# Performance work log

Measured on AMD Instinct MI355X. Metric: run time of the kernel, lower is better.

The kernel has to match this reference:

```python
import jax, jax.numpy as jnp
import numpy as np
import math

B, T, D, N = 4, 2048, 1024, 16
HD = D // N
SCALE = math.sqrt(D)  # source scales by sqrt(d_key) = sqrt(full model dim)
BIG = 1e9

def setup_inputs() -> dict:
    key = jax.random.key(0)
    ks = jax.random.split(key, 11)
    s = 1.0 / math.sqrt(D)
    return {
        "query": jax.random.normal(ks[0], (B, T, D), jnp.float32),
        "key": jax.random.normal(ks[1], (B, T, D), jnp.float32),
        "value": jax.random.normal(ks[2], (B, T, D), jnp.float32),
        "wq_w": jax.random.normal(ks[3], (D, D), jnp.float32) * s,
        "wq_b": jnp.zeros((D,), jnp.float32),
        "wk_w": jax.random.normal(ks[4], (D, D), jnp.float32) * s,
        "wk_b": jnp.zeros((D,), jnp.float32),
        "wv_w": jax.random.normal(ks[5], (D, D), jnp.float32) * s,
        "wv_b": jnp.zeros((D,), jnp.float32),
        "wo_w": jax.random.normal(ks[6], (D, D), jnp.float32) * s,
        "wo_b": jnp.zeros((D,), jnp.float32),
    }

def reference(query, key, value, wq_w, wq_b, wk_w, wk_b, wv_w, wv_b, wo_w, wo_b):
    # projections (torch Linear equiv; weights stored as (in,out))
    q = query @ wq_w + wq_b
    k = key @ wk_w + wk_b
    v = value @ wv_w + wv_b
    # split heads: (B,T,D) -> (B,N,T,HD)
    def split(x):
        return x.reshape(B, T, N, HD).transpose(0, 2, 1, 3)
    q, k, v = split(q), split(k), split(v)
    # dot products (source does elementwise mul+sum == einsum)
    scores = jnp.einsum('bnqd,bnkd->bnqk', q, k)
    # only_attend_front: subtract 1e9 on strict upper triangle
    tri = jnp.triu(jnp.ones((T, T), scores.dtype), 1) * BIG
    scores = scores - tri
    logits = scores / SCALE
    probs = jax.nn.softmax(logits, axis=-1)
    # zero rows where every position is masked (source trick)
    alive = ((scores <= -BIG / 2).sum(-1, keepdims=True) < T).astype(probs.dtype)
    probs = probs * alive
    out = jnp.einsum('bnqk,bnkd->bnqd', probs, v)  # (B,N,T,HD)
    out = out.transpose(0, 2, 1, 3).reshape(B, T, D)
    return out @ wo_w + wo_b
```

## Files before the change

kernel.cpp:

```cpp
#include <hip/hip_runtime.h>
#include <hip/hip_bf16.h>

#define BB 4
#define TT 2048
#define DD 1024
#define NHEAD 16
#define HDIM 64

typedef __bf16 v8bf __attribute__((ext_vector_type(8)));
typedef __bf16 v4bf __attribute__((ext_vector_type(4)));
typedef float  v4f  __attribute__((ext_vector_type(4)));

#define C2SCALE 0.04508422376f

__device__ __forceinline__ void gl2lds16(const void* g, void* l) {
  __builtin_amdgcn_global_load_lds(
      (__attribute__((address_space(1))) const void*)g,
      (__attribute__((address_space(3))) void*)l, 16, 0, 0);
}

__global__ __launch_bounds__(256) void prep(
    const float* __restrict__ qsrc, const float* __restrict__ ksrc,
    const float* __restrict__ vsrc,
    const float* __restrict__ w0, const float* __restrict__ w1,
    const float* __restrict__ w2, const float* __restrict__ w3,
    __bf16* __restrict__ qdst, __bf16* __restrict__ kdst,
    __bf16* __restrict__ vdst,
    __bf16* __restrict__ t0, __bf16* __restrict__ t1,
    __bf16* __restrict__ t2, __bf16* __restrict__ t3) {
  constexpr int STR = 72;
  __shared__ __bf16 sh[64 * STR];
  int bx = blockIdx.x, tid = threadIdx.x;
  if (bx < 1536) {
    int z = bx >> 9, ib = bx & 511;
    const float* src = z == 0 ? qsrc : z == 1 ? ksrc : vsrc;
    __bf16* dst = z == 0 ? qdst : z == 1 ? kdst : vdst;
#pragma unroll
    for (int k = 0; k < 8; ++k) {
      int u = ib * 2048 + k * 256 + tid;
      const float4* s = (const float4*)src + (size_t)u * 2;
      float4 f0 = s[0], f1 = s[1];
      v8bf v;
      v[0] = (__bf16)f0.x; v[1] = (__bf16)f0.y; v[2] = (__bf16)f0.z; v[3] = (__bf16)f0.w;
      v[4] = (__bf16)f1.x; v[5] = (__bf16)f1.y; v[6] = (__bf16)f1.z; v[7] = (__bf16)f1.w;
      *(v8bf*)(dst + (size_t)u * 8) = v;
    }
  } else {
    int idx = bx - 1536;
    int z = idx >> 8;
    const float* W = z == 0 ? w0 : z == 1 ? w1 : z == 2 ? w2 : w3;
    __bf16* Wt = z == 0 ? t0 : z == 1 ? t1 : z == 2 ? t2 : t3;
    int n0 = (idx & 15) * 64, k0 = ((idx >> 4) & 15) * 64;
#pragma unroll
    for (int p = 0; p < 4; ++p) {
      int c = tid + p * 256;
      int r = c >> 4, off = (c & 15) * 4;
      float4 f = *(const float4*)(W + (size_t)(k0 + r) * DD + n0 + off);
      __bf16* d = &sh[r * STR + off];
      d[0] = (__bf16)f.x; d[1] = (__bf16)f.y; d[2] = (__bf16)f.z; d[3] = (__bf16)f.w;
    }
    __syncthreads();
#pragma unroll
    for (int p = 0; p < 2; ++p) {
      int c = tid + p * 256;
      int nr = c >> 3, koff = (c & 7) * 8;
      v8bf v;
#pragma unroll
      for (int j = 0; j < 8; ++j) v[j] = sh[(koff + j) * STR + nr];
      *(v8bf*)(Wt + (size_t)(n0 + nr) * DD + k0 + koff) = v;
    }
  }
}

__device__ __forceinline__ void gemm_core(const __bf16* __restrict__ A,
                                          const __bf16* __restrict__ Wt,
                                          int m0, int n0,
                                          __bf16* ash, __bf16* bsh,
                                          int wave, int lane, int quad, int l15,
                                          v4f acc[4][4]) {
  int wm = (wave & 1) * 64, wn = (wave >> 1) * 64;
  for (int k0 = 0; k0 < DD; k0 += 64) {
    __syncthreads();
#pragma unroll
    for (int i = 0; i < 4; ++i) {
      int c = wave * 256 + i * 64 + lane;
      int row = c >> 3, g = (c & 7) ^ (row & 7);
      gl2lds16(A + (size_t)(m0 + row) * DD + k0 + g * 8, ash + wave * 2048 + i * 512);
      gl2lds16(Wt + (size_t)(n0 + row) * DD + k0 + g * 8, bsh + wave * 2048 + i * 512);
    }
    __syncthreads();
#pragma unroll
    for (int ks = 0; ks < 2; ++ks) {
      int sw = (((ks * 4 + quad) ^ (l15 & 7))) * 8;
      v8bf a[4], b[4];
#pragma unroll
      for (int jm = 0; jm < 4; ++jm) a[jm] = *(v8bf*)&ash[(wm + jm * 16 + l15) * 64 + sw];
#pragma unroll
      for (int jn = 0; jn < 4; ++jn) b[jn] = *(v8bf*)&bsh[(wn + jn * 16 + l15) * 64 + sw];
#pragma unroll
      for (int jm = 0; jm < 4; ++jm)
#pragma unroll
        for (int jn = 0; jn < 4; ++jn)
          acc[jm][jn] = __builtin_amdgcn_mfma_f32_16x16x32_bf16(a[jm], b[jn], acc[jm][jn], 0, 0, 0);
    }
  }
}

__device__ __forceinline__ void swz_tiles(int& m0, int& n0) {
  int lin = blockIdx.x + 8 * blockIdx.y;
  int c = lin & 7, t = lin >> 3;
  n0 = (t & 7) * 128;
  m0 = (c + ((t >> 3) << 3)) * 128;
}

__global__ __launch_bounds__(256) void gemm_qkv(
    const __bf16* __restrict__ Qc, const __bf16* __restrict__ Kc,
    const __bf16* __restrict__ Vc,
    const __bf16* __restrict__ wqT, const __bf16* __restrict__ wkT,
    const __bf16* __restrict__ wvT,
    const float* __restrict__ qb, const float* __restrict__ kb,
    const float* __restrict__ vb,
    __bf16* __restrict__ Qp, __bf16* __restrict__ Kp, __bf16* __restrict__ VTb) {
  __shared__ __bf16 ash[128 * 64];
  __shared__ __bf16 bsh[128 * 64];
  int z = blockIdx.z;
  const __bf16* A  = z == 0 ? Qc : z == 1 ? Kc : Vc;
  const __bf16* Wt = z == 0 ? wqT : z == 1 ? wkT : wvT;
  const float* bias = z == 0 ? qb : z == 1 ? kb : vb;
  int tid = threadIdx.x, wave = tid >> 6, lane = tid & 63;
  int quad = lane >> 4, l15 = lane & 15;
  int m0, n0;
  swz_tiles(m0, n0);
  int wm = (wave & 1) * 64, wn = (wave >> 1) * 64;
  v4f acc[4][4];
#pragma unroll
  for (int jm = 0; jm < 4; ++jm)
#pragma unroll
    for (int jn = 0; jn < 4; ++jn) acc[jm][jn] = (v4f){0.f, 0.f, 0.f, 0.f};

  gemm_core(A, Wt, m0, n0, ash, bsh, wave, lane, quad, l15, acc);

  if (z == 2) {
    int b = m0 >> 11;
    int tbase = (m0 & 2047) + wm;
#pragma unroll
    for (int jn = 0; jn < 4; ++jn) {
      int col = n0 + wn + jn * 16 + l15;
      float bv = bias[col];
      __bf16* rowp = VTb + ((size_t)(b * 16 + (col >> 6)) * 64 + (col & 63)) * TT;
#pragma unroll
      for (int jm = 0; jm < 4; ++jm) {
        v4bf o;
#pragma unroll
        for (int r = 0; r < 4; ++r) o[r] = (__bf16)(acc[jm][jn][r] + bv);
        *(v4bf*)(rowp + tbase + jm * 16 + quad * 4) = o;
      }
    }
  } else {
    __bf16* C = z == 0 ? Qp : Kp;
    float scale = z == 0 ? C2SCALE : 1.0f;
#pragma unroll
    for (int jn = 0; jn < 4; ++jn) {
      int col = n0 + wn + jn * 16 + l15;
      float bv = bias[col];
#pragma unroll
      for (int jm = 0; jm < 4; ++jm) {
#pragma unroll
        for (int r = 0; r < 4; ++r) {
          int row = m0 + wm + jm * 16 + quad * 4 + r;
          C[(size_t)row * DD + col] = (__bf16)((acc[jm][jn][r] + bv) * scale);
        }
      }
    }
  }
}

__global__ __launch_bounds__(256) void gemm_out(const __bf16* __restrict__ A,
                                                const __bf16* __restrict__ Wt,
                                                const float* __restrict__ bias,
                                                float* __restrict__ C) {
  __shared__ __bf16 ash[128 * 64];
  __shared__ __bf16 bsh[128 * 64];
  int tid = threadIdx.x, wave = tid >> 6, lane = tid & 63;
  int quad = lane >> 4, l15 = lane & 15;
  int m0, n0;
  swz_tiles(m0, n0);
  int wm = (wave & 1) * 64, wn = (wave >> 1) * 64;
  v4f acc[4][4];
#pragma unroll
  for (int jm = 0; jm < 4; ++jm)
#pragma unroll
    for (int jn = 0; jn < 4; ++jn) acc[jm][jn] = (v4f){0.f, 0.f, 0.f, 0.f};

  gemm_core(A, Wt, m0, n0, ash, bsh, wave, lane, quad, l15, acc);

#pragma unroll
  for (int jn = 0; jn < 4; ++jn) {
    int col = n0 + wn + jn * 16 + l15;
    float bv = bias[col];
#pragma unroll
    for (int jm = 0; jm < 4; ++jm) {
#pragma unroll
      for (int r = 0; r < 4; ++r) {
        int row = m0 + wm + jm * 16 + quad * 4 + r;
        C[(size_t)row * DD + col] = acc[jm][jn][r] + bv;
      }
    }
  }
}

__global__ __launch_bounds__(256) void attn_bal(const __bf16* __restrict__ Q,
                                                const __bf16* __restrict__ K,
                                                const __bf16* __restrict__ VT,
                                                __bf16* __restrict__ O) {
  __shared__ __bf16 ksh[2][64 * 64];
  __shared__ __bf16 vsh[2][64 * 64];
  __shared__ __bf16 psh[128 * 64];
  int tid = threadIdx.x, wave = tid >> 6, lane = tid & 63;
  int quad = lane >> 4, l15 = lane & 15;
  int swz = l15 & 7;
  int c = blockIdx.x;
  int by = blockIdx.y;
  int bh = c + 8 * (by & 7);
  int qi = 15 - (by >> 3);
  int b = bh >> 4, h = bh & 15;
  const __bf16* Qb = Q + (size_t)(b * TT) * DD + h * HDIM;
  const __bf16* Kb = K + (size_t)(b * TT) * DD + h * HDIM;
  const __bf16* Vb = VT + (size_t)bh * HDIM * TT;
  __bf16* Ob = O + (size_t)(b * TT) * DD + h * HDIM;

  v8bf ones;
#pragma unroll
  for (int j = 0; j < 8; ++j) ones[j] = (__bf16)1.0f;

  int q0 = qi * 128;
  int ktiles = 2 * qi + 2;

#pragma unroll
  for (int i = 0; i < 4; ++i) {
    int cc = wave * 256 + i * 64 + lane;
    int row = cc >> 3, g = (cc & 7) ^ (row & 7);
    gl2lds16(Qb + (size_t)(q0 + row) * DD + g * 8, psh + wave * 2048 + i * 512);
  }
#pragma unroll
  for (int i = 0; i < 2; ++i) {
    int cc = wave * 128 + i * 64 + lane;
    int row = cc >> 3, g = (cc & 7) ^ (row & 7);
    gl2lds16(Kb + (size_t)row * DD + g * 8, &ksh[0][wave * 1024 + i * 512]);
    gl2lds16(Vb + (size_t)row * TT + g * 8, &vsh[0][wave * 1024 + i * 512]);
  }
  __builtin_amdgcn_s_waitcnt(0);
  __syncthreads();

  v8bf qf[2][2];
#pragma unroll
  for (int set = 0; set < 2; ++set)
#pragma unroll
    for (int ks = 0; ks < 2; ++ks)
      qf[set][ks] = *(v8bf*)&psh[(wave * 32 + set * 16 + l15) * 64 + ((ks * 4 + quad) ^ swz) * 8];

  int qg[2] = {q0 + wave * 32 + l15, q0 + wave * 32 + 16 + l15};
  v4f oacc[2][4], lracc[2];
#pragma unroll
  for (int set = 0; set < 2; ++set) {
    lracc[set] = (v4f){0.f, 0.f, 0.f, 0.f};
#pragma unroll
    for (int jm = 0; jm < 4; ++jm) oacc[set][jm] = (v4f){0.f, 0.f, 0.f, 0.f};
  }

  int pbuf = 0;
  for (int kt = 0; kt < ktiles; ++kt) {
    if (kt + 1 < ktiles) {
      int k0n = (kt + 1) * 64;
#pragma unroll
      for (int i = 0; i < 2; ++i) {
        int cc = wave * 128 + i * 64 + lane;
        int row = cc >> 3, g = (cc & 7) ^ (row & 7);
        gl2lds16(Kb + (size_t)(k0n + row) * DD + g * 8, &ksh[pbuf ^ 1][wave * 1024 + i * 512]);
        gl2lds16(Vb + (size_t)row * TT + k0n + g * 8, &vsh[pbuf ^ 1][wave * 1024 + i * 512]);
      }
    }
    int k0 = kt * 64;
    const __bf16* kshp = &ksh[pbuf][0];
    const __bf16* vshp = &vsh[pbuf][0];

    v4f s[2][4];
#pragma unroll
    for (int set = 0; set < 2; ++set)
#pragma unroll
      for (int jf = 0; jf < 4; ++jf) s[set][jf] = (v4f){0.f, 0.f, 0.f, 0.f};
    __builtin_amdgcn_s_setprio(1);
#pragma unroll
    for (int ks = 0; ks < 2; ++ks) {
      int sw = ((ks * 4 + quad) ^ swz) * 8;
#pragma unroll
      for (int jf = 0; jf < 4; ++jf) {
        v8bf kf = *(v8bf*)&kshp[(jf * 16 + l15) * 64 + sw];
        s[0][jf] = __builtin_amdgcn_mfma_f32_16x16x32_bf16(kf, qf[0][ks], s[0][jf], 0, 0, 0);
        s[1][jf] = __builtin_amdgcn_mfma_f32_16x16x32_bf16(kf, qf[1][ks], s[1][jf], 0, 0, 0);
      }
    }
    __builtin_amdgcn_s_setprio(0);

    bool diag = (kt >= 2 * qi);
#pragma unroll
    for (int set = 0; set < 2; ++set) {
      int qrow = wave * 32 + set * 16 + l15;
      __bf16* prow = &psh[qrow * 64];
#pragma unroll
      for (int jf = 0; jf < 4; ++jf) {
        v4bf pk;
#pragma unroll
        for (int r = 0; r < 4; ++r) {
          float p = __builtin_amdgcn_exp2f(s[set][jf][r]);
          if (diag) {
            int kg = k0 + jf * 16 + quad * 4 + r;
            if (kg > qg[set]) p = 0.f;
          }
          pk[r] = (__bf16)p;
        }
        int chunk = jf * 2 + (quad >> 1);
        *(v4bf*)&prow[(chunk ^ swz) * 8 + (quad & 1) * 4] = pk;
      }
    }

    __builtin_amdgcn_s_setprio(1);
#pragma unroll
    for (int ks = 0; ks < 2; ++ks) {
      int sw = ((ks * 4 + quad) ^ swz) * 8;
      v8bf pb0 = *(v8bf*)&psh[(wave * 32 + l15) * 64 + sw];
      v8bf pb1 = *(v8bf*)&psh[(wave * 32 + 16 + l15) * 64 + sw];
      lracc[0] = __builtin_amdgcn_mfma_f32_16x16x32_bf16(ones, pb0, lracc[0], 0, 0, 0);
      lracc[1] = __builtin_amdgcn_mfma_f32_16x16x32_bf16(ones, pb1, lracc[1], 0, 0, 0);
#pragma unroll
      for (int jm = 0; jm < 4; ++jm) {
        v8bf vf = *(v8bf*)&vshp[(jm * 16 + l15) * 64 + sw];
        oacc[0][jm] = __builtin_amdgcn_mfma_f32_16x16x32_bf16(vf, pb0, oacc[0][jm], 0, 0, 0);
        oacc[1][jm] = __builtin_amdgcn_mfma_f32_16x16x32_bf16(vf, pb1, oacc[1][jm], 0, 0, 0);
      }
    }
    __builtin_amdgcn_s_setprio(0);

    __builtin_amdgcn_s_waitcnt(0);
    __syncthreads();
    pbuf ^= 1;
  }

#pragma unroll
  for (int set = 0; set < 2; ++set) {
    float inv = 1.0f / lracc[set][0];
    int q = q0 + wave * 32 + set * 16 + l15;
#pragma unroll
    for (int jm = 0; jm < 4; ++jm) {
      v4bf o;
#pragma unroll
      for (int r = 0; r < 4; ++r) o[r] = (__bf16)(oacc[set][jm][r] * inv);
      *(v4bf*)(Ob + (size_t)q * DD + jm * 16 + quad * 4) = o;
    }
  }
}

extern "C" void kernel_launch(void* const* d_in, const int* in_sizes, int n_in,
                              void* d_out, int out_size, void* d_ws, size_t ws_size,
                              hipStream_t stream) {
  const float* query = (const float*)d_in[0];
  const float* key_  = (const float*)d_in[1];
  const float* value = (const float*)d_in[2];
  const float* wq_w = (const float*)d_in[3];
  const float* wq_b = (const float*)d_in[4];
  const float* wk_w = (const float*)d_in[5];
  const float* wk_b = (const float*)d_in[6];
  const float* wv_w = (const float*)d_in[7];
  const float* wv_b = (const float*)d_in[8];
  const float* wo_w = (const float*)d_in[9];
  const float* wo_b = (const float*)d_in[10];

  char* ws = (char*)d_ws;
  const size_t MB = (size_t)1 << 20;
  __bf16* wqT = (__bf16*)(ws + 0 * MB);
  __bf16* wkT = (__bf16*)(ws + 2 * MB);
  __bf16* wvT = (__bf16*)(ws + 4 * MB);
  __bf16* woT = (__bf16*)(ws + 6 * MB);
  __bf16* Qc  = (__bf16*)(ws + 8 * MB);
  __bf16* Kc  = (__bf16*)(ws + 24 * MB);
  __bf16* Vc  = (__bf16*)(ws + 40 * MB);
  __bf16* Qp  = (__bf16*)(ws + 56 * MB);
  __bf16* Kp  = (__bf16*)(ws + 72 * MB);
  __bf16* VTb = (__bf16*)(ws + 88 * MB);
  __bf16* Ab  = (__bf16*)(ws + 8 * MB);
  float* out = (float*)d_out;

  dim3 tb(256);
  prep<<<dim3(2560), tb, 0, stream>>>(query, key_, value, wq_w, wk_w, wv_w, wo_w,
                                      Qc, Kc, Vc, wqT, wkT, wvT, woT);
  gemm_qkv<<<dim3(8, 64, 3), tb, 0, stream>>>(Qc, Kc, Vc, wqT, wkT, wvT,
                                              wq_b, wk_b, wv_b, Qp, Kp, VTb);
  attn_bal<<<dim3(8, 128), tb, 0, stream>>>(Qp, Kp, VTb, Ab);
  gemm_out<<<dim3(8, 64), tb, 0, stream>>>(Ab, woT, wo_b, out);
}
```

Measured before the change: 308.2 us.

## Enlarge attention query tile to 256 rows per block with dynamic LDS

The attention kernel now processes 256 query rows per block instead of 128, so each wave handles 64 rows (four 16-row sets). Each K/V tile loaded into LDS is reused across twice as many queries. The grid is halved and the query-tile ordering changes to alternate long and short causal rows. The kernel moves to 64KB of dynamic shared memory with a launch bound of two blocks per CU. This raises register and LDS pressure and leaves fewer blocks to balance the causal work.

```diff
diff --git a/kernel.cpp b/kernel.cpp
--- a/kernel.cpp
+++ b/kernel.cpp
@@ -209,20 +209,22 @@
   }
 }
 
-__global__ __launch_bounds__(256) void attn_bal(const __bf16* __restrict__ Q,
-                                                const __bf16* __restrict__ K,
-                                                const __bf16* __restrict__ VT,
-                                                __bf16* __restrict__ O) {
-  __shared__ __bf16 ksh[2][64 * 64];
-  __shared__ __bf16 vsh[2][64 * 64];
-  __shared__ __bf16 psh[128 * 64];
+__global__ __launch_bounds__(256, 2) void attn_bal(const __bf16* __restrict__ Q,
+                                                   const __bf16* __restrict__ K,
+                                                   const __bf16* __restrict__ VT,
+                                                   __bf16* __restrict__ O) {
+  extern __shared__ __bf16 lds[];
+  __bf16* ksh = lds;
+  __bf16* vsh = lds + 8192;
+  __bf16* psh = lds + 16384;
   int tid = threadIdx.x, wave = tid >> 6, lane = tid & 63;
   int quad = lane >> 4, l15 = lane & 15;
   int swz = l15 & 7;
   int c = blockIdx.x;
-  int by = blockIdx.y;
-  int bh = c + 8 * (by & 7);
-  int qi = 15 - (by >> 3);
+  int y = blockIdx.y;
+  int bh = c + 8 * (y & 7);
+  int yy = y >> 3;
+  int qi = yy < 4 ? 7 - yy : yy - 4;
   int b = bh >> 4, h = bh & 15;
   const __bf16* Qb = Q + (size_t)(b * TT) * DD + h * HDIM;
   const __bf16* Kb = K + (size_t)(b * TT) * DD + h * HDIM;
@@ -233,36 +235,38 @@
 #pragma unroll
   for (int j = 0; j < 8; ++j) ones[j] = (__bf16)1.0f;
 
-  int q0 = qi * 128;
-  int ktiles = 2 * qi + 2;
-
-#pragma unroll
-  for (int i = 0; i < 4; ++i) {
-    int cc = wave * 256 + i * 64 + lane;
+  int q0 = qi * 256;
+  int ktiles = 4 * qi + 4;
+
+#pragma unroll
+  for (int i = 0; i < 8; ++i) {
+    int cc = wave * 512 + i * 64 + lane;
     int row = cc >> 3, g = (cc & 7) ^ (row & 7);
-    gl2lds16(Qb + (size_t)(q0 + row) * DD + g * 8, psh + wave * 2048 + i * 512);
+    gl2lds16(Qb + (size_t)(q0 + row) * DD + g * 8, psh + wave * 4096 + i * 512);
   }
 #pragma unroll
   for (int i = 0; i < 2; ++i) {
     int cc = wave * 128 + i * 64 + lane;
     int row = cc >> 3, g = (cc & 7) ^ (row & 7);
-    gl2lds16(Kb + (size_t)row * DD + g * 8, &ksh[0][wave * 1024 + i * 512]);
-    gl2lds16(Vb + (size_t)row * TT + g * 8, &vsh[0][wave * 1024 + i * 512]);
+    gl2lds16(Kb + (size_t)row * DD + g * 8, ksh + wave * 1024 + i * 512);
+    gl2lds16(Vb + (size_t)row * TT + g * 8, vsh + wave * 1024 + i * 512);
   }
   __builtin_amdgcn_s_waitcnt(0);
   __syncthreads();
 
-  v8bf qf[2][2];
-#pragma unroll
-  for (int set = 0; set < 2; ++set)
+  v8bf qf[4][2];
+#pragma unroll
+  for (int set = 0; set < 4; ++set)
 #pragma unroll
     for (int ks = 0; ks < 2; ++ks)
-      qf[set][ks] = *(v8bf*)&psh[(wave * 32 + set * 16 + l15) * 64 + ((ks * 4 + quad) ^ swz) * 8];
-
-  int qg[2] = {q0 + wave * 32 + l15, q0 + wave * 32 + 16 + l15};
-  v4f oacc[2][4], lracc[2];
-#pragma unroll
-  for (int set = 0; set < 2; ++set) {
+      qf[set][ks] = *(v8bf*)&psh[(wave * 64 + set * 16 + l15) * 64 + ((ks * 4 + quad) ^ swz) * 8];
+
+  int qg[4];
+#pragma unroll
+  for (int set = 0; set < 4; ++set) qg[set] = q0 + wave * 64 + set * 16 + l15;
+  v4f oacc[4][4], lracc[4];
+#pragma unroll
+  for (int set = 0; set < 4; ++set) {
     lracc[set] = (v4f){0.f, 0.f, 0.f, 0.f};
 #pragma unroll
     for (int jm = 0; jm < 4; ++jm) oacc[set][jm] = (v4f){0.f, 0.f, 0.f, 0.f};
@@ -276,51 +280,63 @@
       for (int i = 0; i < 2; ++i) {
         int cc = wave * 128 + i * 64 + lane;
         int row = cc >> 3, g = (cc & 7) ^ (row & 7);
-        gl2lds16(Kb + (size_t)(k0n + row) * DD + g * 8, &ksh[pbuf ^ 1][wave * 1024 + i * 512]);
-        gl2lds16(Vb + (size_t)row * TT + k0n + g * 8, &vsh[pbuf ^ 1][wave * 1024 + i * 512]);
+        gl2lds16(Kb + (size_t)(k0n + row) * DD + g * 8,
+                 ksh + (pbuf ^ 1) * 4096 + wave * 1024 + i * 512);
+        gl2lds16(Vb + (size_t)row * TT + k0n + g * 8,
+                 vsh + (pbuf ^ 1) * 4096 + wave * 1024 + i * 512);
       }
     }
     int k0 = kt * 64;
-    const __bf16* kshp = &ksh[pbuf][0];
-    const __bf16* vshp = &vsh[pbuf][0];
-
-    v4f s[2][4];
-#pragma unroll
-    for (int set = 0; set < 2; ++set)
-#pragma unroll
-      for (int jf = 0; jf < 4; ++jf) s[set][jf] = (v4f){0.f, 0.f, 0.f, 0.f};
-    __builtin_amdgcn_s_setprio(1);
+    const __bf16* kshp = ksh + pbuf * 4096;
+    const __bf16* vshp = vsh + pbuf * 4096;
+
+    v8bf kf[2][4];
 #pragma unroll
     for (int ks = 0; ks < 2; ++ks) {
       int sw = ((ks * 4 + quad) ^ swz) * 8;
 #pragma unroll
-      for (int jf = 0; jf < 4; ++jf) {
-        v8bf kf = *(v8bf*)&kshp[(jf * 16 + l15) * 64 + sw];
-        s[0][jf] = __builtin_amdgcn_mfma_f32_16x16x32_bf16(kf, qf[0][ks], s[0][jf], 0, 0, 0);
-        s[1][jf] = __builtin_amdgcn_mfma_f32_16x16x32_bf16(kf, qf[1][ks], s[1][jf], 0, 0, 0);
-      }
-    }
-    __builtin_amdgcn_s_setprio(0);
-
-    bool diag = (kt >= 2 * qi);
-#pragma unroll
-    for (int set = 0; set < 2; ++set) {
-      int qrow = wave * 32 + set * 16 + l15;
-      __bf16* prow = &psh[qrow * 64];
-#pragma unroll
-      for (int jf = 0; jf < 4; ++jf) {
-        v4bf pk;
-#pragma unroll
-        for (int r = 0; r < 4; ++r) {
-          float p = __builtin_amdgcn_exp2f(s[set][jf][r]);
-          if (diag) {
-            int kg = k0 + jf * 16 + quad * 4 + r;
-            if (kg > qg[set]) p = 0.f;
+      for (int jf = 0; jf < 4; ++jf)
+        kf[ks][jf] = *(v8bf*)&kshp[(jf * 16 + l15) * 64 + sw];
+    }
+
+    bool diag = (kt >= 4 * qi);
+#pragma unroll
+    for (int sp = 0; sp < 2; ++sp) {
+      v4f s[2][4];
+#pragma unroll
+      for (int ss = 0; ss < 2; ++ss)
+#pragma unroll
+        for (int jf = 0; jf < 4; ++jf) s[ss][jf] = (v4f){0.f, 0.f, 0.f, 0.f};
+      __builtin_amdgcn_s_setprio(1);
+#pragma unroll
+      for (int ks = 0; ks < 2; ++ks)
+#pragma unroll
+        for (int jf = 0; jf < 4; ++jf) {
+          s[0][jf] = __builtin_amdgcn_mfma_f32_16x16x32_bf16(kf[ks][jf], qf[sp * 2][ks], s[0][jf], 0, 0, 0);
+          s[1][jf] = __builtin_amdgcn_mfma_f32_16x16x32_bf16(kf[ks][jf], qf[sp * 2 + 1][ks], s[1][jf], 0, 0, 0);
+        }
+      __builtin_amdgcn_s_setprio(0);
+
+#pragma unroll
+      for (int ss = 0; ss < 2; ++ss) {
+        int set = sp * 2 + ss;
+        int qrow = wave * 64 + set * 16 + l15;
+        __bf16* prow = &psh[qrow * 64];
+#pragma unroll
+        for (int jf = 0; jf < 4; ++jf) {
+          v4bf pk;
+#pragma unroll
+          for (int r = 0; r < 4; ++r) {
+            float p = __builtin_amdgcn_exp2f(s[ss][jf][r]);
+            if (diag) {
+              int kg = k0 + jf * 16 + quad * 4 + r;
+              if (kg > qg[set]) p = 0.f;
+            }
+            pk[r] = (__bf16)p;
           }
-          pk[r] = (__bf16)p;
+          int chunk = jf * 2 + (quad >> 1);
+          *(v4bf*)&prow[(chunk ^ swz) * 8 + (quad & 1) * 4] = pk;
         }
-        int chunk = jf * 2 + (quad >> 1);
-        *(v4bf*)&prow[(chunk ^ swz) * 8 + (quad & 1) * 4] = pk;
       }
     }
 
@@ -328,15 +344,19 @@
 #pragma unroll
     for (int ks = 0; ks < 2; ++ks) {
       int sw = ((ks * 4 + quad) ^ swz) * 8;
-      v8bf pb0 = *(v8bf*)&psh[(wave * 32 + l15) * 64 + sw];
-      v8bf pb1 = *(v8bf*)&psh[(wave * 32 + 16 + l15) * 64 + sw];
-      lracc[0] = __builtin_amdgcn_mfma_f32_16x16x32_bf16(ones, pb0, lracc[0], 0, 0, 0);
-      lracc[1] = __builtin_amdgcn_mfma_f32_16x16x32_bf16(ones, pb1, lracc[1], 0, 0, 0);
+      v8bf pb[4];
+#pragma unroll
+      for (int set = 0; set < 4; ++set)
+        pb[set] = *(v8bf*)&psh[(wave * 64 + set * 16 + l15) * 64 + sw];
+#pragma unroll
+      for (int set = 0; set < 4; ++set)
+        lracc[set] = __builtin_amdgcn_mfma_f32_16x16x32_bf16(ones, pb[set], lracc[set], 0, 0, 0);
 #pragma unroll
       for (int jm = 0; jm < 4; ++jm) {
         v8bf vf = *(v8bf*)&vshp[(jm * 16 + l15) * 64 + sw];
-        oacc[0][jm] = __builtin_amdgcn_mfma_f32_16x16x32_bf16(vf, pb0, oacc[0][jm], 0, 0, 0);
-        oacc[1][jm] = __builtin_amdgcn_mfma_f32_16x16x32_bf16(vf, pb1, oacc[1][jm], 0, 0, 0);
+#pragma unroll
+        for (int set = 0; set < 4; ++set)
+          oacc[set][jm] = __builtin_amdgcn_mfma_f32_16x16x32_bf16(vf, pb[set], oacc[set][jm], 0, 0, 0);
       }
     }
     __builtin_amdgcn_s_setprio(0);
@@ -347,9 +367,9 @@
   }
 
 #pragma unroll
-  for (int set = 0; set < 2; ++set) {
+  for (int set = 0; set < 4; ++set) {
     float inv = 1.0f / lracc[set][0];
-    int q = q0 + wave * 32 + set * 16 + l15;
+    int q = q0 + wave * 64 + set * 16 + l15;
 #pragma unroll
     for (int jm = 0; jm < 4; ++jm) {
       v4bf o;
@@ -390,11 +410,18 @@
   __bf16* Ab  = (__bf16*)(ws + 8 * MB);
   float* out = (float*)d_out;
 
+  static int attr_done = 0;
+  if (!attr_done) {
+    hipFuncSetAttribute((const void*)attn_bal,
+                        hipFuncAttributeMaxDynamicSharedMemorySize, 65536);
+    attr_done = 1;
+  }
+
   dim3 tb(256);
   prep<<<dim3(2560), tb, 0, stream>>>(query, key_, value, wq_w, wk_w, wv_w, wo_w,
                                       Qc, Kc, Vc, wqT, wkT, wvT, woT);
   gemm_qkv<<<dim3(8, 64, 3), tb, 0, stream>>>(Qc, Kc, Vc, wqT, wkT, wvT,
                                               wq_b, wk_b, wv_b, Qp, Kp, VTb);
-  attn_bal<<<dim3(8, 128), tb, 0, stream>>>(Qp, Kp, VTb, Ab);
+  attn_bal<<<dim3(8, 64), tb, 65536, stream>>>(Qp, Kp, VTb, Ab);
   gemm_out<<<dim3(8, 64), tb, 0, stream>>>(Ab, woT, wo_b, out);
 }
```

Result: slower. 318.6 us (+3.4%).
